# Performance work log

Hardware: AMD Instinct MI355X
Metric: run time of the kernel (lower is better)

The kernel has to match this reference:

```python
import jax, jax.numpy as jnp
import numpy as np

N_F, N_C = 100000, 25000          # fine / coarse node counts
C_IN, C_OUT = 128, 128
E_POOL, E = 200000, 400000        # pooling edges, coarse point-point edges


def setup_inputs() -> dict:
    key = jax.random.key(0)
    ks = jax.random.split(key, 12)
    x = jax.random.normal(ks[0], (N_F, C_IN), jnp.float32)
    # pooling edges: src in fine graph, dst in coarse graph
    pool_src = jax.random.randint(ks[1], (E_POOL,), 0, N_F, dtype=jnp.int64)
    pool_dst = jax.random.randint(ks[2], (E_POOL,), 0, N_C, dtype=jnp.int64)
    pool_edge_index = jnp.stack([pool_src, pool_dst])
    pool_edge_attr = jax.random.uniform(ks[3], (E_POOL,), jnp.float32)
    # coarse point-point edges
    src = jax.random.randint(ks[4], (E,), 0, N_C, dtype=jnp.int64)
    dst = jax.random.randint(ks[5], (E,), 0, N_C, dtype=jnp.int64)
    edge_index = jnp.stack([src, dst])
    edge_attr = jax.random.uniform(ks[6], (E,), jnp.float32)
    s_in = 1.0 / np.sqrt(C_IN).astype(np.float32)
    s_out = 1.0 / np.sqrt(C_OUT).astype(np.float32)
    W1_root = jax.random.normal(ks[7], (C_IN, C_OUT), jnp.float32) * s_in
    W1_nb = jax.random.normal(ks[8], (C_IN, C_OUT), jnp.float32) * s_in
    b1 = jnp.zeros((C_OUT,), jnp.float32)
    W2_root = jax.random.normal(ks[9], (C_OUT, C_OUT), jnp.float32) * s_out
    W2_nb = jax.random.normal(ks[10], (C_OUT, C_OUT), jnp.float32) * s_out
    b2 = jnp.zeros((C_OUT,), jnp.float32)
    return {
        "x": x,
        "pool_edge_index": pool_edge_index,
        "pool_edge_attr": pool_edge_attr,
        "edge_index": edge_index,
        "edge_attr": edge_attr,
        "W1_root": W1_root, "W1_nb": W1_nb, "b1": b1,
        "W2_root": W2_root, "W2_nb": W2_nb, "b2": b2,
        "n_coarse": N_C,
    }


def _graph_conv(h, edge_index, edge_attr, W_root, W_nb, b, n_nodes):
    # GraphConv with edge weights: out = h @ W_root + scatter_add(w_e * (h[src] @ W_nb), dst) + b
    msg = edge_attr[:, None] * (h[edge_index[0]] @ W_nb)          # [E, C_out]
    agg = jax.ops.segment_sum(msg, edge_index[1], num_segments=n_nodes)
    return h @ W_root + agg + b


def reference(x, pool_edge_index, pool_edge_attr, edge_index, edge_attr,
              W1_root, W1_nb, b1, W2_root, W2_nb, b2, n_coarse):
    # CustomPoolingAdd: weighted scatter-add fine -> coarse
    pooled = jax.ops.segment_sum(pool_edge_attr[:, None] * x[pool_edge_index[0]],
                                 pool_edge_index[1], num_segments=n_coarse)  # [N_c, C_in]
    h = _graph_conv(pooled, edge_index, edge_attr, W1_root, W1_nb, b1, n_coarse)
    h = _graph_conv(h, edge_index, edge_attr, W2_root, W2_nb, b2, n_coarse)
    return h
```

## Files before the change

### kernel.cpp

```cpp
#include <hip/hip_runtime.h>

typedef __attribute__((ext_vector_type(8))) short   short8;
typedef __attribute__((ext_vector_type(8))) __bf16  bf16x8;
typedef __attribute__((ext_vector_type(4))) float   f32x4;

__device__ __forceinline__ float bf2f(unsigned short u) {
    union { unsigned int i; float f; } v; v.i = ((unsigned int)u) << 16; return v.f;
}
__device__ __forceinline__ unsigned short f2bf(float f) {
    union { float f; unsigned int i; } v; v.f = f;
    unsigned int r = v.i + 0x7fffu + ((v.i >> 16) & 1u);
    return (unsigned short)(r >> 16);
}

__device__ __forceinline__ int load_idx(const void* p, int is64, long long i) {
    return is64 ? (int)((const long long*)p)[i] : ((const int*)p)[i];
}
__device__ __forceinline__ float load_f(const void* p, int isbf, long long i) {
    return isbf ? bf2f(((const unsigned short*)p)[i]) : ((const float*)p)[i];
}

__device__ __forceinline__ int self_is64(const int* p) {
    int lane = threadIdx.x & 63;
    unsigned long long b = __ballot(p[2 * lane + 1] != 0);
    return b == 0ull;
}
__device__ __forceinline__ int self_isbf(const unsigned int* p) {
    int lane = threadIdx.x & 63;
    unsigned int lo = p[lane] & 0xFFFFu;
    int e = (int)((lo >> 7) & 0xFF);
    int ok = (lo == 0u) || (e >= 88 && e <= 141);
    return (__ballot(!ok) == 0ull) ? 1 : 0;
}

__global__ void detect_kernel(const int* __restrict__ pei, const int* __restrict__ ei,
                              const unsigned int* f0, const unsigned int* f1,
                              const unsigned int* f2, const unsigned int* f3,
                              const unsigned int* f4, const unsigned int* f5,
                              const unsigned int* f6, const unsigned int* f7,
                              const unsigned int* f8,
                              int* __restrict__ flags) {
    int lane = threadIdx.x & 63;
    unsigned long long ba = __ballot(pei[2 * lane + 1] != 0);
    unsigned long long bb = __ballot(ei[2 * lane + 1] != 0);
    const unsigned int* fa[9] = {f0, f1, f2, f3, f4, f5, f6, f7, f8};
    int bf[9];
    #pragma unroll
    for (int t = 0; t < 9; t++) {
        unsigned int lo = fa[t][lane] & 0xFFFFu;
        int e = (int)((lo >> 7) & 0xFF);
        int ok = (lo == 0u) || (e >= 88 && e <= 141);
        bf[t] = (__ballot(!ok) == 0ull) ? 1 : 0;
    }
    if (lane == 0) {
        flags[0] = (ba == 0ull);
        flags[1] = (bb == 0ull);
        #pragma unroll
        for (int t = 0; t < 9; t++) flags[2 + t] = bf[t];
    }
}

#define PBKT_CAP 32
#define CBKT_CAP 64
#define OVF_CAP 4096

__global__ void fillpack_kernel(const void* __restrict__ pei, const void* __restrict__ pattr,
                                const void* __restrict__ ei, const void* __restrict__ eattr,
                                int* __restrict__ pcnt, int2* __restrict__ pbkt,
                                int* __restrict__ povfc, int4* __restrict__ povf,
                                int* __restrict__ ccnt, int2* __restrict__ cbkt,
                                int* __restrict__ covfc, int4* __restrict__ covf,
                                int Ep, int Ec, int gE,
                                const void* __restrict__ w1r, const void* __restrict__ w1n,
                                const void* __restrict__ w2r, const void* __restrict__ w2n,
                                unsigned short* __restrict__ wpack,
                                const void* __restrict__ x, unsigned short* __restrict__ xb,
                                long long elemsX) {
    int bid = (int)blockIdx.x;
    if (bid >= gE + 256) {
        int xisbf = self_isbf((const unsigned int*)x);
        if (xisbf) return;
        long long gid = (long long)(bid - gE - 256) * 256 + threadIdx.x;
        long long row = gid >> 3;
        int part = (int)(gid & 7);
        long long NF = elemsX >> 7;
        if (row >= NF) return;
        const float4* src = (const float4*)((const float*)x + row * 128 + part * 16);
        float4 a = src[0], b = src[1], c = src[2], d = src[3];
        uint4 o0, o1;
        o0.x = (unsigned int)f2bf(a.x) | ((unsigned int)f2bf(a.y) << 16);
        o0.y = (unsigned int)f2bf(a.z) | ((unsigned int)f2bf(a.w) << 16);
        o0.z = (unsigned int)f2bf(b.x) | ((unsigned int)f2bf(b.y) << 16);
        o0.w = (unsigned int)f2bf(b.z) | ((unsigned int)f2bf(b.w) << 16);
        o1.x = (unsigned int)f2bf(c.x) | ((unsigned int)f2bf(c.y) << 16);
        o1.y = (unsigned int)f2bf(c.z) | ((unsigned int)f2bf(c.w) << 16);
        o1.z = (unsigned int)f2bf(d.x) | ((unsigned int)f2bf(d.y) << 16);
        o1.w = (unsigned int)f2bf(d.z) | ((unsigned int)f2bf(d.w) << 16);
        uint4* dst = (uint4*)(xb + row * 128 + part * 16);
        dst[0] = o0; dst[1] = o1;
        return;
    }
    if (bid >= gE) {
        int gid = (bid - gE) * 256 + threadIdx.x;
        int layer = gid >> 15;
        int r = gid & 32767;
        int j = r & 7, lane = (r >> 3) & 63, ch = (r >> 9) & 7, ct = (r >> 12) & 7;
        int n = ct * 16 + (lane & 15);
        int k = ch * 32 + (lane >> 4) * 8 + j;
        const void* w;
        if (layer == 0) w = (k < 128) ? w1r : w1n;
        else            w = (k < 128) ? w2r : w2n;
        int fs = self_isbf((const unsigned int*)w);
        float v = load_f(w, fs, (long long)(k & 127) * 128 + n);
        wpack[gid] = f2bf(v);
        return;
    }
    long long g = (long long)bid * 256 + threadIdx.x;
    if (g < Ep) {
        int is64 = self_is64((const int*)pei);
        int abf = self_isbf((const unsigned int*)pattr);
        int s = load_idx(pei, is64, g);
        int d = load_idx(pei, is64, (long long)Ep + g);
        float w = load_f(pattr, abf, g);
        int pos = atomicAdd(&pcnt[d], 1);
        if (pos < PBKT_CAP) {
            pbkt[(long long)d * PBKT_CAP + pos] = make_int2(s, __float_as_int(w));
        } else {
            int oi = atomicAdd(povfc, 1);
            if (oi < OVF_CAP) povf[oi] = make_int4(s, __float_as_int(w), d, 0);
        }
    } else if (g - Ep < Ec) {
        long long e = g - Ep;
        int is64 = self_is64((const int*)ei);
        int abf = self_isbf((const unsigned int*)eattr);
        int s = load_idx(ei, is64, e);
        int d = load_idx(ei, is64, (long long)Ec + e);
        float w = load_f(eattr, abf, e);
        int pos = atomicAdd(&ccnt[d], 1);
        if (pos < CBKT_CAP) {
            cbkt[(long long)d * CBKT_CAP + pos] = make_int2(s, __float_as_int(w));
        } else {
            int oi = atomicAdd(covfc, 1);
            if (oi < OVF_CAP) covf[oi] = make_int4(s, __float_as_int(w), d, 0);
        }
    }
}

__global__ void gatherx_kernel(const void* __restrict__ x,
                               const unsigned short* __restrict__ xb, int haveXb,
                               const int* __restrict__ cnt,
                               const int2* __restrict__ bkt,
                               const int* __restrict__ ovfc,
                               const int4* __restrict__ ovf,
                               unsigned short* __restrict__ out, int NC) {
    int d = blockIdx.x * 4 + (threadIdx.x >> 6);
    if (d >= NC) return;
    int lane = threadIdx.x & 63;
    int j1 = cnt[d]; if (j1 > PBKT_CAP) j1 = PBKT_CAP;
    const int2* row = bkt + (long long)d * PBKT_CAP;
    float ax = 0.f, ay = 0.f;
    int xisbf = self_isbf((const unsigned int*)x);
    if (xisbf || haveXb) {
        const unsigned int* uin = xisbf ? (const unsigned int*)x : (const unsigned int*)xb;
        int j = 0;
        for (; j + 4 <= j1; j += 4) {
            int2 e0 = row[j], e1 = row[j + 1], e2 = row[j + 2], e3 = row[j + 3];
            unsigned int v0 = uin[(long long)e0.x * 64 + lane];
            unsigned int v1 = uin[(long long)e1.x * 64 + lane];
            unsigned int v2 = uin[(long long)e2.x * 64 + lane];
            unsigned int v3 = uin[(long long)e3.x * 64 + lane];
            ax += __int_as_float(e0.y) * bf2f((unsigned short)v0)
                + __int_as_float(e1.y) * bf2f((unsigned short)v1)
                + __int_as_float(e2.y) * bf2f((unsigned short)v2)
                + __int_as_float(e3.y) * bf2f((unsigned short)v3);
            ay += __int_as_float(e0.y) * bf2f((unsigned short)(v0 >> 16))
                + __int_as_float(e1.y) * bf2f((unsigned short)(v1 >> 16))
                + __int_as_float(e2.y) * bf2f((unsigned short)(v2 >> 16))
                + __int_as_float(e3.y) * bf2f((unsigned short)(v3 >> 16));
        }
        for (; j < j1; j++) {
            int2 e = row[j];
            float w = __int_as_float(e.y);
            unsigned int v = uin[(long long)e.x * 64 + lane];
            ax += w * bf2f((unsigned short)v);
            ay += w * bf2f((unsigned short)(v >> 16));
        }
        int novf = *ovfc;
        if (novf > 0) {
            if (novf > OVF_CAP) novf = OVF_CAP;
            for (int k = 0; k < novf; k++) {
                int4 e = ovf[k];
                if (e.z == d) {
                    float w = __int_as_float(e.y);
                    unsigned int v = uin[(long long)e.x * 64 + lane];
                    ax += w * bf2f((unsigned short)v);
                    ay += w * bf2f((unsigned short)(v >> 16));
                }
            }
        }
    } else {
        const float* fin = (const float*)x;
        int c0 = lane * 2;
        int j = 0;
        for (; j + 4 <= j1; j += 4) {
            int2 e0 = row[j], e1 = row[j + 1], e2 = row[j + 2], e3 = row[j + 3];
            float2 v0 = *(const float2*)(fin + (long long)e0.x * 128 + c0);
            float2 v1 = *(const float2*)(fin + (long long)e1.x * 128 + c0);
            float2 v2 = *(const float2*)(fin + (long long)e2.x * 128 + c0);
            float2 v3 = *(const float2*)(fin + (long long)e3.x * 128 + c0);
            ax += __int_as_float(e0.y) * v0.x + __int_as_float(e1.y) * v1.x
                + __int_as_float(e2.y) * v2.x + __int_as_float(e3.y) * v3.x;
            ay += __int_as_float(e0.y) * v0.y + __int_as_float(e1.y) * v1.y
                + __int_as_float(e2.y) * v2.y + __int_as_float(e3.y) * v3.y;
        }
        for (; j < j1; j++) {
            int2 e = row[j];
            float w = __int_as_float(e.y);
            float2 v = *(const float2*)(fin + (long long)e.x * 128 + c0);
            ax += w * v.x; ay += w * v.y;
        }
        int novf = *ovfc;
        if (novf > 0) {
            if (novf > OVF_CAP) novf = OVF_CAP;
            for (int k = 0; k < novf; k++) {
                int4 e = ovf[k];
                if (e.z == d) {
                    float w = __int_as_float(e.y);
                    float2 v = *(const float2*)(fin + (long long)e.x * 128 + c0);
                    ax += w * v.x; ay += w * v.y;
                }
            }
        }
    }
    unsigned int o = (unsigned int)f2bf(ax) | ((unsigned int)f2bf(ay) << 16);
    ((unsigned int*)out)[(long long)d * 64 + lane] = o;
}

__global__ void gatherb_kernel(const unsigned short* __restrict__ in,
                               const int* __restrict__ cnt,
                               const int2* __restrict__ bkt, int cap,
                               const int* __restrict__ ovfc,
                               const int4* __restrict__ ovf,
                               unsigned short* __restrict__ out, int NC) {
    int d = blockIdx.x * 4 + (threadIdx.x >> 6);
    if (d >= NC) return;
    int lane = threadIdx.x & 63;
    int j1 = cnt[d]; if (j1 > cap) j1 = cap;
    const int2* row = bkt + (long long)d * cap;
    float ax = 0.f, ay = 0.f;
    const unsigned int* uin = (const unsigned int*)in;
    int j = 0;
    for (; j + 8 <= j1; j += 8) {
        int2 e0 = row[j], e1 = row[j + 1], e2 = row[j + 2], e3 = row[j + 3];
        int2 e4 = row[j + 4], e5 = row[j + 5], e6 = row[j + 6], e7 = row[j + 7];
        unsigned int v0 = uin[(long long)e0.x * 64 + lane];
        unsigned int v1 = uin[(long long)e1.x * 64 + lane];
        unsigned int v2 = uin[(long long)e2.x * 64 + lane];
        unsigned int v3 = uin[(long long)e3.x * 64 + lane];
        unsigned int v4 = uin[(long long)e4.x * 64 + lane];
        unsigned int v5 = uin[(long long)e5.x * 64 + lane];
        unsigned int v6 = uin[(long long)e6.x * 64 + lane];
        unsigned int v7 = uin[(long long)e7.x * 64 + lane];
        ax += __int_as_float(e0.y) * bf2f((unsigned short)v0)
            + __int_as_float(e1.y) * bf2f((unsigned short)v1)
            + __int_as_float(e2.y) * bf2f((unsigned short)v2)
            + __int_as_float(e3.y) * bf2f((unsigned short)v3)
            + __int_as_float(e4.y) * bf2f((unsigned short)v4)
            + __int_as_float(e5.y) * bf2f((unsigned short)v5)
            + __int_as_float(e6.y) * bf2f((unsigned short)v6)
            + __int_as_float(e7.y) * bf2f((unsigned short)v7);
        ay += __int_as_float(e0.y) * bf2f((unsigned short)(v0 >> 16))
            + __int_as_float(e1.y) * bf2f((unsigned short)(v1 >> 16))
            + __int_as_float(e2.y) * bf2f((unsigned short)(v2 >> 16))
            + __int_as_float(e3.y) * bf2f((unsigned short)(v3 >> 16))
            + __int_as_float(e4.y) * bf2f((unsigned short)(v4 >> 16))
            + __int_as_float(e5.y) * bf2f((unsigned short)(v5 >> 16))
            + __int_as_float(e6.y) * bf2f((unsigned short)(v6 >> 16))
            + __int_as_float(e7.y) * bf2f((unsigned short)(v7 >> 16));
    }
    for (; j + 4 <= j1; j += 4) {
        int2 e0 = row[j], e1 = row[j + 1], e2 = row[j + 2], e3 = row[j + 3];
        unsigned int v0 = uin[(long long)e0.x * 64 + lane];
        unsigned int v1 = uin[(long long)e1.x * 64 + lane];
        unsigned int v2 = uin[(long long)e2.x * 64 + lane];
        unsigned int v3 = uin[(long long)e3.x * 64 + lane];
        ax += __int_as_float(e0.y) * bf2f((unsigned short)v0)
            + __int_as_float(e1.y) * bf2f((unsigned short)v1)
            + __int_as_float(e2.y) * bf2f((unsigned short)v2)
            + __int_as_float(e3.y) * bf2f((unsigned short)v3);
        ay += __int_as_float(e0.y) * bf2f((unsigned short)(v0 >> 16))
            + __int_as_float(e1.y) * bf2f((unsigned short)(v1 >> 16))
            + __int_as_float(e2.y) * bf2f((unsigned short)(v2 >> 16))
            + __int_as_float(e3.y) * bf2f((unsigned short)(v3 >> 16));
    }
    for (; j < j1; j++) {
        int2 e = row[j];
        float w = __int_as_float(e.y);
        unsigned int v = uin[(long long)e.x * 64 + lane];
        ax += w * bf2f((unsigned short)v);
        ay += w * bf2f((unsigned short)(v >> 16));
    }
    int novf = *ovfc;
    if (novf > 0) {
        if (novf > OVF_CAP) novf = OVF_CAP;
        for (int k = 0; k < novf; k++) {
            int4 e = ovf[k];
            if (e.z == d) {
                float w = __int_as_float(e.y);
                unsigned int v = uin[(long long)e.x * 64 + lane];
                ax += w * bf2f((unsigned short)v);
                ay += w * bf2f((unsigned short)(v >> 16));
            }
        }
    }
    unsigned int o = (unsigned int)f2bf(ax) | ((unsigned int)f2bf(ay) << 16);
    ((unsigned int*)out)[(long long)d * 64 + lane] = o;
}

__global__ __launch_bounds__(256, 4)
void gemm_mfma_kernel(const unsigned short* __restrict__ H,
                      const unsigned short* __restrict__ G,
                      const unsigned short* __restrict__ wpack,
                      const void* __restrict__ bias,
                      float* __restrict__ outF, unsigned short* __restrict__ outB,
                      int NC) {
    __shared__ unsigned short ldsA[64 * 264];
    int tid = threadIdx.x;
    long long r0 = (long long)blockIdx.x * 64;
    for (int i = tid; i < 4096; i += 256) {
        int mat = i >> 11;
        int flat = i & 2047;
        int row = flat >> 5;
        int c4 = flat & 31;
        long long r = r0 + row;
        const unsigned short* srcp = mat ? G : H;
        uint2 v = make_uint2(0u, 0u);
        if (r < NC) v = *(const uint2*)(srcp + r * 128 + c4 * 4);
        *(uint2*)&ldsA[row * 264 + mat * 128 + c4 * 4] = v;
    }
    __syncthreads();

    int wave = tid >> 6, lane = tid & 63;
    int m = lane & 15, quad = lane >> 4;
    int arow = wave * 16 + m;

    bf16x8 a[8];
    #pragma unroll
    for (int ch = 0; ch < 8; ch++) {
        short8 av = *(const short8*)&ldsA[arow * 264 + ch * 32 + quad * 8];
        a[ch] = __builtin_bit_cast(bf16x8, av);
    }

    f32x4 acc[8];
    #pragma unroll
    for (int ct = 0; ct < 8; ct++) acc[ct] = (f32x4){0.f, 0.f, 0.f, 0.f};

    #pragma unroll
    for (int ct = 0; ct < 8; ct++) {
        #pragma unroll
        for (int ch = 0; ch < 8; ch++) {
            short8 bv = *(const short8*)(wpack + ((ct * 8 + ch) * 64 + lane) * 8);
            acc[ct] = __builtin_amdgcn_mfma_f32_16x16x32_bf16(
                a[ch], __builtin_bit_cast(bf16x8, bv), acc[ct], 0, 0, 0);
        }
    }

    int bbf = self_isbf((const unsigned int*)bias);
    #pragma unroll
    for (int ct = 0; ct < 8; ct++) {
        int n = ct * 16 + m;
        float bv = load_f(bias, bbf, n);
        #pragma unroll
        for (int r = 0; r < 4; r++) {
            long long rr = r0 + wave * 16 + quad * 4 + r;
            if (rr < NC) {
                float val = acc[ct][r] + bv;
                if (outF) outF[rr * 128 + n] = val;
                else      outB[rr * 128 + n] = f2bf(val);
            }
        }
    }
}

__global__ void pool_scatter_kernel(const void* __restrict__ x, const void* __restrict__ pei,
                                    const void* __restrict__ pattr, const int* __restrict__ flags,
                                    float* __restrict__ pooled, int Ep, int CI) {
    int c = blockIdx.y * blockDim.x + threadIdx.x;
    if (c >= CI) return;
    int e = blockIdx.x;
    int is64 = flags[0], xbf = flags[2], abf = flags[3];
    int s = load_idx(pei, is64, e);
    int d = load_idx(pei, is64, (long long)Ep + e);
    float w = load_f(pattr, abf, e);
    float v = load_f(x, xbf, (long long)s * CI + c);
    atomicAdd(&pooled[(long long)d * CI + c], w * v);
}

__global__ void conv_scatter_kernel(const float* __restrict__ t, const void* __restrict__ ei,
                                    const void* __restrict__ attr, const int* __restrict__ flags,
                                    float* __restrict__ outacc, int Ec, int CO) {
    int c = blockIdx.y * blockDim.x + threadIdx.x;
    if (c >= CO) return;
    int e = blockIdx.x;
    int is64 = flags[1], abf = flags[4];
    int s = load_idx(ei, is64, e);
    int d = load_idx(ei, is64, (long long)Ec + e);
    float w = load_f(attr, abf, e);
    atomicAdd(&outacc[(long long)d * CO + c], w * t[(long long)s * CO + c]);
}

__global__ void gemm_kernel(const float* H, const void* __restrict__ Wr,
                            const void* __restrict__ Wn, const void* __restrict__ bias,
                            const int* __restrict__ flags, int fWr, int fWn, int fB,
                            float* out_root, float* out_t, int NC, int CI, int CO) {
    __shared__ float lds[4][1024];
    int wave = threadIdx.x >> 6;
    int lane = threadIdx.x & 63;
    int r = blockIdx.x * 4 + wave;
    if (r < NC) {
        const float* hrow = H + (long long)r * CI;
        for (int k = lane; k < CI; k += 64) lds[wave][k] = hrow[k];
    }
    __syncthreads();
    if (r >= NC) return;
    int wrbf = flags[fWr], wnbf = flags[fWn], bbf = flags[fB];
    for (int c0 = lane * 2; c0 < CO; c0 += 128) {
        int two = (c0 + 1 < CO);
        float ar0 = 0.f, ar1 = 0.f, an0 = 0.f, an1 = 0.f;
        for (int k = 0; k < CI; k++) {
            float h = lds[wave][k];
            ar0 += h * load_f(Wr, wrbf, (long long)k * CO + c0);
            an0 += h * load_f(Wn, wnbf, (long long)k * CO + c0);
            if (two) {
                ar1 += h * load_f(Wr, wrbf, (long long)k * CO + c0 + 1);
                an1 += h * load_f(Wn, wnbf, (long long)k * CO + c0 + 1);
            }
        }
        long long o = (long long)r * CO + c0;
        out_root[o] = ar0 + load_f(bias, bbf, c0);
        out_t[o] = an0;
        if (two) {
            out_root[o + 1] = ar1 + load_f(bias, bbf, c0 + 1);
            out_t[o + 1] = an1;
        }
    }
}

__global__ void to_out_kernel(const float* __restrict__ in, float* __restrict__ out, long long n) {
    long long stride = (long long)gridDim.x * blockDim.x;
    for (long long i = (long long)blockIdx.x * blockDim.x + threadIdx.x; i < n; i += stride)
        out[i] = in[i];
}

extern "C" void kernel_launch(void* const* d_in, const int* in_sizes, int n_in,
                              void* d_out, int out_size, void* d_ws, size_t ws_size,
                              hipStream_t stream) {
    const void* x = d_in[0]; const void* pei = d_in[1]; const void* pattr = d_in[2];
    const void* ei = d_in[3]; const void* eattr = d_in[4];
    const void* w1r = d_in[5]; const void* w1n = d_in[6]; const void* b1 = d_in[7];
    const void* w2r = d_in[8]; const void* w2n = d_in[9]; const void* b2 = d_in[10];

    long long CO = in_sizes[7];
    long long CI = CO > 0 ? in_sizes[5] / CO : 0;
    long long Ep = in_sizes[2];
    long long Ec = in_sizes[4];
    long long NC = CO > 0 ? (long long)out_size / CO : 0;
    int sane = (CO > 0 && CI > 0 && CI <= 1024 && CO <= 1024 &&
                CI * CO == in_sizes[5] && NC * CO == out_size &&
                Ep > 0 && Ec > 0 && in_sizes[0] % CI == 0);
    if (!sane) { CO = 128; CI = 128; Ep = 200000; Ec = 400000; NC = 25000; }

    char* ws = (char*)d_ws;

    if (CI == 128 && CO == 128) {
        long long elemsX = in_sizes[0];
        size_t off = 0;
        unsigned short* bufP = (unsigned short*)(ws + off); off += (size_t)NC * 128 * 2;
        unsigned short* bufH = (unsigned short*)(ws + off); off += (size_t)NC * 128 * 2;
        unsigned short* bufG = (unsigned short*)(ws + off); off += (size_t)NC * 128 * 2;
        unsigned short* wpack = (unsigned short*)(ws + off); off += 65536 * 2;
        int* pcnt  = (int*)(ws + off); off += NC * 4;
        int* ccnt  = (int*)(ws + off); off += NC * 4;
        int* povfc = (int*)(ws + off); off += 4;
        int* covfc = (int*)(ws + off); off += 4;
        off = (off + 15) & ~(size_t)15;
        int4* povf = (int4*)(ws + off); off += (size_t)OVF_CAP * 16;
        int4* covf = (int4*)(ws + off); off += (size_t)OVF_CAP * 16;
        int2* pbkt = (int2*)(ws + off); off += (size_t)NC * PBKT_CAP * 8;
        int2* cbkt = (int2*)(ws + off); off += (size_t)NC * CBKT_CAP * 8;
        off = (off + 15) & ~(size_t)15;
        unsigned short* xb = (unsigned short*)(ws + off);
        size_t xbBytes = (size_t)elemsX * 2;
        int haveXb = (off + xbBytes <= ws_size) ? 1 : 0;

        hipMemsetAsync(pcnt, 0, (2 * NC + 2) * 4, stream);

        int gE = (int)((Ep + Ec + 255) / 256);
        int gConv = haveXb ? (int)((elemsX / 16 + 255) / 256) : 0;
        fillpack_kernel<<<gE + 256 + gConv, 256, 0, stream>>>(
            pei, pattr, ei, eattr,
            pcnt, pbkt, povfc, povf,
            ccnt, cbkt, covfc, covf,
            (int)Ep, (int)Ec, gE,
            w1r, w1n, w2r, w2n, wpack,
            x, xb, elemsX);

        int gN4 = (int)((NC + 3) / 4);
        int gN64 = (int)((NC + 63) / 64);
        gatherx_kernel<<<gN4, 256, 0, stream>>>(x, xb, haveXb, pcnt, pbkt, povfc, povf,
                                                bufP, (int)NC);
        gatherb_kernel<<<gN4, 256, 0, stream>>>(bufP, ccnt, cbkt, CBKT_CAP, covfc, covf,
                                                bufG, (int)NC);
        gemm_mfma_kernel<<<gN64, 256, 0, stream>>>(bufP, bufG, wpack, b1,
                                                   nullptr, bufH, (int)NC);
        gatherb_kernel<<<gN4, 256, 0, stream>>>(bufH, ccnt, cbkt, CBKT_CAP, covfc, covf,
                                                bufG, (int)NC);
        gemm_mfma_kernel<<<gN64, 256, 0, stream>>>(bufH, bufG, wpack + 32768, b2,
                                                   (float*)d_out, nullptr, (int)NC);
        return;
    }

    size_t szP = (size_t)NC * CI * sizeof(float);
    size_t szO = (size_t)NC * CO * sizeof(float);
    float *bufP, *bufA, *bufB, *bufC; int* flags;
    if (CI == CO) {
        bufP = (float*)ws; bufA = (float*)(ws + szP);
        bufB = bufP; bufC = bufA;
        flags = (int*)(ws + szP + szO);
    } else {
        bufP = (float*)ws; bufA = (float*)(ws + szP);
        bufB = (float*)(ws + szP + szO); bufC = (float*)(ws + szP + 2 * szO);
        flags = (int*)(ws + szP + 3 * szO);
    }
    detect_kernel<<<1, 64, 0, stream>>>(
        (const int*)pei, (const int*)ei,
        (const unsigned int*)x, (const unsigned int*)pattr, (const unsigned int*)eattr,
        (const unsigned int*)w1r, (const unsigned int*)w1n, (const unsigned int*)b1,
        (const unsigned int*)w2r, (const unsigned int*)w2n, (const unsigned int*)b2,
        flags);
    hipMemsetAsync(bufP, 0, szP, stream);
    int blkP = (CI % 64 == 0 && CI <= 256) ? (int)CI : 256;
    int blkC = (CO % 64 == 0 && CO <= 256) ? (int)CO : 256;
    dim3 gP((unsigned)Ep, (unsigned)((CI + blkP - 1) / blkP));
    dim3 gC((unsigned)Ec, (unsigned)((CO + blkC - 1) / blkC));
    int gG = (int)((NC + 3) / 4);
    pool_scatter_kernel<<<gP, blkP, 0, stream>>>(x, pei, pattr, flags, bufP, (int)Ep, (int)CI);
    if (CI == CO) {
        gemm_kernel<<<gG, 256, 0, stream>>>(bufP, w1r, w1n, b1, flags, 5, 6, 7,
                                            bufA, bufP, (int)NC, (int)CI, (int)CO);
        conv_scatter_kernel<<<gC, blkC, 0, stream>>>(bufP, ei, eattr, flags, bufA, (int)Ec, (int)CO);
        gemm_kernel<<<gG, 256, 0, stream>>>(bufA, w2r, w2n, b2, flags, 8, 9, 10,
                                            bufP, bufA, (int)NC, (int)CO, (int)CO);
        conv_scatter_kernel<<<gC, blkC, 0, stream>>>(bufA, ei, eattr, flags, bufP, (int)Ec, (int)CO);
        to_out_kernel<<<4096, 256, 0, stream>>>(bufP, (float*)d_out, NC * CO);
    } else {
        gemm_kernel<<<gG, 256, 0, stream>>>(bufP, w1r, w1n, b1, flags, 5, 6, 7,
                                            bufA, bufB, (int)NC, (int)CI, (int)CO);
        conv_scatter_kernel<<<gC, blkC, 0, stream>>>(bufB, ei, eattr, flags, bufA, (int)Ec, (int)CO);
        gemm_kernel<<<gG, 256, 0, stream>>>(bufA, w2r, w2n, b2, flags, 8, 9, 10,
                                            bufB, bufC, (int)NC, (int)CO, (int)CO);
        conv_scatter_kernel<<<gC, blkC, 0, stream>>>(bufC, ei, eattr, flags, bufB, (int)Ec, (int)CO);
        to_out_kernel<<<4096, 256, 0, stream>>>(bufB, (float*)d_out, NC * CO);
    }
}
```

Baseline: 231.8 us.

## Fuse neighbor gather into MFMA GEMM and drop x bf16 pre-conversion

Merges the per-layer neighbor aggregation kernel into the GEMM kernel, so each block gathers its 64 rows' neighbor sums straight into LDS next to the root features and no longer writes and rereads an intermediate G buffer. It also removes the pass that converted x to bf16 inside the fill kernel, so gatherx now reads fp32 x directly when x is not already bf16. The trade-off is less parallelism in the fused gather (64 rows per block, 16 per wave, run serially), and gatherx moves twice the bytes on the fp32 path.

```diff
diff --git a/kernel.cpp b/kernel.cpp
--- a/kernel.cpp
+++ b/kernel.cpp
@@ -73,33 +73,8 @@
                                 int Ep, int Ec, int gE,
                                 const void* __restrict__ w1r, const void* __restrict__ w1n,
                                 const void* __restrict__ w2r, const void* __restrict__ w2n,
-                                unsigned short* __restrict__ wpack,
-                                const void* __restrict__ x, unsigned short* __restrict__ xb,
-                                long long elemsX) {
+                                unsigned short* __restrict__ wpack) {
     int bid = (int)blockIdx.x;
-    if (bid >= gE + 256) {
-        int xisbf = self_isbf((const unsigned int*)x);
-        if (xisbf) return;
-        long long gid = (long long)(bid - gE - 256) * 256 + threadIdx.x;
-        long long row = gid >> 3;
-        int part = (int)(gid & 7);
-        long long NF = elemsX >> 7;
-        if (row >= NF) return;
-        const float4* src = (const float4*)((const float*)x + row * 128 + part * 16);
-        float4 a = src[0], b = src[1], c = src[2], d = src[3];
-        uint4 o0, o1;
-        o0.x = (unsigned int)f2bf(a.x) | ((unsigned int)f2bf(a.y) << 16);
-        o0.y = (unsigned int)f2bf(a.z) | ((unsigned int)f2bf(a.w) << 16);
-        o0.z = (unsigned int)f2bf(b.x) | ((unsigned int)f2bf(b.y) << 16);
-        o0.w = (unsigned int)f2bf(b.z) | ((unsigned int)f2bf(b.w) << 16);
-        o1.x = (unsigned int)f2bf(c.x) | ((unsigned int)f2bf(c.y) << 16);
-        o1.y = (unsigned int)f2bf(c.z) | ((unsigned int)f2bf(c.w) << 16);
-        o1.z = (unsigned int)f2bf(d.x) | ((unsigned int)f2bf(d.y) << 16);
-        o1.w = (unsigned int)f2bf(d.z) | ((unsigned int)f2bf(d.w) << 16);
-        uint4* dst = (uint4*)(xb + row * 128 + part * 16);
-        dst[0] = o0; dst[1] = o1;
-        return;
-    }
     if (bid >= gE) {
         int gid = (bid - gE) * 256 + threadIdx.x;
         int layer = gid >> 15;
@@ -147,7 +122,6 @@
 }
 
 __global__ void gatherx_kernel(const void* __restrict__ x,
-                               const unsigned short* __restrict__ xb, int haveXb,
                                const int* __restrict__ cnt,
                                const int2* __restrict__ bkt,
                                const int* __restrict__ ovfc,
@@ -160,8 +134,8 @@
     const int2* row = bkt + (long long)d * PBKT_CAP;
     float ax = 0.f, ay = 0.f;
     int xisbf = self_isbf((const unsigned int*)x);
-    if (xisbf || haveXb) {
-        const unsigned int* uin = xisbf ? (const unsigned int*)x : (const unsigned int*)xb;
+    if (xisbf) {
+        const unsigned int* uin = (const unsigned int*)x;
         int j = 0;
         for (; j + 4 <= j1; j += 4) {
             int2 e0 = row[j], e1 = row[j + 1], e2 = row[j + 2], e3 = row[j + 3];
@@ -236,111 +210,108 @@
     ((unsigned int*)out)[(long long)d * 64 + lane] = o;
 }
 
-__global__ void gatherb_kernel(const unsigned short* __restrict__ in,
-                               const int* __restrict__ cnt,
-                               const int2* __restrict__ bkt, int cap,
-                               const int* __restrict__ ovfc,
-                               const int4* __restrict__ ovf,
-                               unsigned short* __restrict__ out, int NC) {
-    int d = blockIdx.x * 4 + (threadIdx.x >> 6);
-    if (d >= NC) return;
-    int lane = threadIdx.x & 63;
-    int j1 = cnt[d]; if (j1 > cap) j1 = cap;
-    const int2* row = bkt + (long long)d * cap;
-    float ax = 0.f, ay = 0.f;
-    const unsigned int* uin = (const unsigned int*)in;
-    int j = 0;
-    for (; j + 8 <= j1; j += 8) {
-        int2 e0 = row[j], e1 = row[j + 1], e2 = row[j + 2], e3 = row[j + 3];
-        int2 e4 = row[j + 4], e5 = row[j + 5], e6 = row[j + 6], e7 = row[j + 7];
-        unsigned int v0 = uin[(long long)e0.x * 64 + lane];
-        unsigned int v1 = uin[(long long)e1.x * 64 + lane];
-        unsigned int v2 = uin[(long long)e2.x * 64 + lane];
-        unsigned int v3 = uin[(long long)e3.x * 64 + lane];
-        unsigned int v4 = uin[(long long)e4.x * 64 + lane];
-        unsigned int v5 = uin[(long long)e5.x * 64 + lane];
-        unsigned int v6 = uin[(long long)e6.x * 64 + lane];
-        unsigned int v7 = uin[(long long)e7.x * 64 + lane];
-        ax += __int_as_float(e0.y) * bf2f((unsigned short)v0)
-            + __int_as_float(e1.y) * bf2f((unsigned short)v1)
-            + __int_as_float(e2.y) * bf2f((unsigned short)v2)
-            + __int_as_float(e3.y) * bf2f((unsigned short)v3)
-            + __int_as_float(e4.y) * bf2f((unsigned short)v4)
-            + __int_as_float(e5.y) * bf2f((unsigned short)v5)
-            + __int_as_float(e6.y) * bf2f((unsigned short)v6)
-            + __int_as_float(e7.y) * bf2f((unsigned short)v7);
-        ay += __int_as_float(e0.y) * bf2f((unsigned short)(v0 >> 16))
-            + __int_as_float(e1.y) * bf2f((unsigned short)(v1 >> 16))
-            + __int_as_float(e2.y) * bf2f((unsigned short)(v2 >> 16))
-            + __int_as_float(e3.y) * bf2f((unsigned short)(v3 >> 16))
-            + __int_as_float(e4.y) * bf2f((unsigned short)(v4 >> 16))
-            + __int_as_float(e5.y) * bf2f((unsigned short)(v5 >> 16))
-            + __int_as_float(e6.y) * bf2f((unsigned short)(v6 >> 16))
-            + __int_as_float(e7.y) * bf2f((unsigned short)(v7 >> 16));
-    }
-    for (; j + 4 <= j1; j += 4) {
-        int2 e0 = row[j], e1 = row[j + 1], e2 = row[j + 2], e3 = row[j + 3];
-        unsigned int v0 = uin[(long long)e0.x * 64 + lane];
-        unsigned int v1 = uin[(long long)e1.x * 64 + lane];
-        unsigned int v2 = uin[(long long)e2.x * 64 + lane];
-        unsigned int v3 = uin[(long long)e3.x * 64 + lane];
-        ax += __int_as_float(e0.y) * bf2f((unsigned short)v0)
-            + __int_as_float(e1.y) * bf2f((unsigned short)v1)
-            + __int_as_float(e2.y) * bf2f((unsigned short)v2)
-            + __int_as_float(e3.y) * bf2f((unsigned short)v3);
-        ay += __int_as_float(e0.y) * bf2f((unsigned short)(v0 >> 16))
-            + __int_as_float(e1.y) * bf2f((unsigned short)(v1 >> 16))
-            + __int_as_float(e2.y) * bf2f((unsigned short)(v2 >> 16))
-            + __int_as_float(e3.y) * bf2f((unsigned short)(v3 >> 16));
-    }
-    for (; j < j1; j++) {
-        int2 e = row[j];
-        float w = __int_as_float(e.y);
-        unsigned int v = uin[(long long)e.x * 64 + lane];
-        ax += w * bf2f((unsigned short)v);
-        ay += w * bf2f((unsigned short)(v >> 16));
-    }
-    int novf = *ovfc;
-    if (novf > 0) {
-        if (novf > OVF_CAP) novf = OVF_CAP;
-        for (int k = 0; k < novf; k++) {
-            int4 e = ovf[k];
-            if (e.z == d) {
+__global__ __launch_bounds__(256, 4)
+void gathergemm_kernel(const unsigned short* __restrict__ H,
+                       const int* __restrict__ cnt,
+                       const int2* __restrict__ bkt, int cap,
+                       const int* __restrict__ ovfc,
+                       const int4* __restrict__ ovf,
+                       const unsigned short* __restrict__ wpack,
+                       const void* __restrict__ bias,
+                       float* __restrict__ outF, unsigned short* __restrict__ outB,
+                       int NC) {
+    __shared__ unsigned short ldsA[64 * 264];
+    int tid = threadIdx.x;
+    long long r0 = (long long)blockIdx.x * 64;
+
+    for (int i = tid; i < 2048; i += 256) {
+        int row = i >> 5;
+        int c4 = i & 31;
+        long long r = r0 + row;
+        uint2 v = make_uint2(0u, 0u);
+        if (r < NC) v = *(const uint2*)(H + r * 128 + c4 * 4);
+        *(uint2*)&ldsA[row * 264 + c4 * 4] = v;
+    }
+
+    int wave = tid >> 6, lane = tid & 63;
+    const unsigned int* uin = (const unsigned int*)H;
+    for (int t = 0; t < 16; t++) {
+        int row = wave * 16 + t;
+        long long d = r0 + row;
+        float ax = 0.f, ay = 0.f;
+        if (d < NC) {
+            int j1 = cnt[d]; if (j1 > cap) j1 = cap;
+            const int2* brow = bkt + d * cap;
+            int j = 0;
+            for (; j + 8 <= j1; j += 8) {
+                int2 e0 = brow[j],     e1 = brow[j + 1], e2 = brow[j + 2], e3 = brow[j + 3];
+                int2 e4 = brow[j + 4], e5 = brow[j + 5], e6 = brow[j + 6], e7 = brow[j + 7];
+                unsigned int v0 = uin[(long long)e0.x * 64 + lane];
+                unsigned int v1 = uin[(long long)e1.x * 64 + lane];
+                unsigned int v2 = uin[(long long)e2.x * 64 + lane];
+                unsigned int v3 = uin[(long long)e3.x * 64 + lane];
+                unsigned int v4 = uin[(long long)e4.x * 64 + lane];
+                unsigned int v5 = uin[(long long)e5.x * 64 + lane];
+                unsigned int v6 = uin[(long long)e6.x * 64 + lane];
+                unsigned int v7 = uin[(long long)e7.x * 64 + lane];
+                ax += __int_as_float(e0.y) * bf2f((unsigned short)v0)
+                    + __int_as_float(e1.y) * bf2f((unsigned short)v1)
+                    + __int_as_float(e2.y) * bf2f((unsigned short)v2)
+                    + __int_as_float(e3.y) * bf2f((unsigned short)v3)
+                    + __int_as_float(e4.y) * bf2f((unsigned short)v4)
+                    + __int_as_float(e5.y) * bf2f((unsigned short)v5)
+                    + __int_as_float(e6.y) * bf2f((unsigned short)v6)
+                    + __int_as_float(e7.y) * bf2f((unsigned short)v7);
+                ay += __int_as_float(e0.y) * bf2f((unsigned short)(v0 >> 16))
+                    + __int_as_float(e1.y) * bf2f((unsigned short)(v1 >> 16))
+                    + __int_as_float(e2.y) * bf2f((unsigned short)(v2 >> 16))
+                    + __int_as_float(e3.y) * bf2f((unsigned short)(v3 >> 16))
+                    + __int_as_float(e4.y) * bf2f((unsigned short)(v4 >> 16))
+                    + __int_as_float(e5.y) * bf2f((unsigned short)(v5 >> 16))
+                    + __int_as_float(e6.y) * bf2f((unsigned short)(v6 >> 16))
+                    + __int_as_float(e7.y) * bf2f((unsigned short)(v7 >> 16));
+            }
+            for (; j + 4 <= j1; j += 4) {
+                int2 e0 = brow[j], e1 = brow[j + 1], e2 = brow[j + 2], e3 = brow[j + 3];
+                unsigned int v0 = uin[(long long)e0.x * 64 + lane];
+                unsigned int v1 = uin[(long long)e1.x * 64 + lane];
+                unsigned int v2 = uin[(long long)e2.x * 64 + lane];
+                unsigned int v3 = uin[(long long)e3.x * 64 + lane];
+                ax += __int_as_float(e0.y) * bf2f((unsigned short)v0)
+                    + __int_as_float(e1.y) * bf2f((unsigned short)v1)
+                    + __int_as_float(e2.y) * bf2f((unsigned short)v2)
+                    + __int_as_float(e3.y) * bf2f((unsigned short)v3);
+                ay += __int_as_float(e0.y) * bf2f((unsigned short)(v0 >> 16))
+                    + __int_as_float(e1.y) * bf2f((unsigned short)(v1 >> 16))
+                    + __int_as_float(e2.y) * bf2f((unsigned short)(v2 >> 16))
+                    + __int_as_float(e3.y) * bf2f((unsigned short)(v3 >> 16));
+            }
+            for (; j < j1; j++) {
+                int2 e = brow[j];
                 float w = __int_as_float(e.y);
                 unsigned int v = uin[(long long)e.x * 64 + lane];
                 ax += w * bf2f((unsigned short)v);
                 ay += w * bf2f((unsigned short)(v >> 16));
             }
-        }
-    }
-    unsigned int o = (unsigned int)f2bf(ax) | ((unsigned int)f2bf(ay) << 16);
-    ((unsigned int*)out)[(long long)d * 64 + lane] = o;
-}
-
-__global__ __launch_bounds__(256, 4)
-void gemm_mfma_kernel(const unsigned short* __restrict__ H,
-                      const unsigned short* __restrict__ G,
-                      const unsigned short* __restrict__ wpack,
-                      const void* __restrict__ bias,
-                      float* __restrict__ outF, unsigned short* __restrict__ outB,
-                      int NC) {
-    __shared__ unsigned short ldsA[64 * 264];
-    int tid = threadIdx.x;
-    long long r0 = (long long)blockIdx.x * 64;
-    for (int i = tid; i < 4096; i += 256) {
-        int mat = i >> 11;
-        int flat = i & 2047;
-        int row = flat >> 5;
-        int c4 = flat & 31;
-        long long r = r0 + row;
-        const unsigned short* srcp = mat ? G : H;
-        uint2 v = make_uint2(0u, 0u);
-        if (r < NC) v = *(const uint2*)(srcp + r * 128 + c4 * 4);
-        *(uint2*)&ldsA[row * 264 + mat * 128 + c4 * 4] = v;
+            int novf = *ovfc;
+            if (novf > 0) {
+                if (novf > OVF_CAP) novf = OVF_CAP;
+                for (int k = 0; k < novf; k++) {
+                    int4 e = ovf[k];
+                    if (e.z == d) {
+                        float w = __int_as_float(e.y);
+                        unsigned int v = uin[(long long)e.x * 64 + lane];
+                        ax += w * bf2f((unsigned short)v);
+                        ay += w * bf2f((unsigned short)(v >> 16));
+                    }
+                }
+            }
+        }
+        *(unsigned int*)&ldsA[row * 264 + 128 + lane * 2] =
+            (unsigned int)f2bf(ax) | ((unsigned int)f2bf(ay) << 16);
     }
     __syncthreads();
 
-    int wave = tid >> 6, lane = tid & 63;
     int m = lane & 15, quad = lane >> 4;
     int arow = wave * 16 + m;
 
@@ -473,11 +444,9 @@
     char* ws = (char*)d_ws;
 
     if (CI == 128 && CO == 128) {
-        long long elemsX = in_sizes[0];
         size_t off = 0;
         unsigned short* bufP = (unsigned short*)(ws + off); off += (size_t)NC * 128 * 2;
         unsigned short* bufH = (unsigned short*)(ws + off); off += (size_t)NC * 128 * 2;
-        unsigned short* bufG = (unsigned short*)(ws + off); off += (size_t)NC * 128 * 2;
         unsigned short* wpack = (unsigned short*)(ws + off); off += 65536 * 2;
         int* pcnt  = (int*)(ws + off); off += NC * 4;
         int* ccnt  = (int*)(ws + off); off += NC * 4;
@@ -488,35 +457,25 @@
         int4* covf = (int4*)(ws + off); off += (size_t)OVF_CAP * 16;
         int2* pbkt = (int2*)(ws + off); off += (size_t)NC * PBKT_CAP * 8;
         int2* cbkt = (int2*)(ws + off); off += (size_t)NC * CBKT_CAP * 8;
-        off = (off + 15) & ~(size_t)15;
-        unsigned short* xb = (unsigned short*)(ws + off);
-        size_t xbBytes = (size_t)elemsX * 2;
-        int haveXb = (off + xbBytes <= ws_size) ? 1 : 0;
 
         hipMemsetAsync(pcnt, 0, (2 * NC + 2) * 4, stream);
 
         int gE = (int)((Ep + Ec + 255) / 256);
-        int gConv = haveXb ? (int)((elemsX / 16 + 255) / 256) : 0;
-        fillpack_kernel<<<gE + 256 + gConv, 256, 0, stream>>>(
+        fillpack_kernel<<<gE + 256, 256, 0, stream>>>(
             pei, pattr, ei, eattr,
             pcnt, pbkt, povfc, povf,
             ccnt, cbkt, covfc, covf,
             (int)Ep, (int)Ec, gE,
-            w1r, w1n, w2r, w2n, wpack,
-            x, xb, elemsX);
+            w1r, w1n, w2r, w2n, wpack);
 
         int gN4 = (int)((NC + 3) / 4);
         int gN64 = (int)((NC + 63) / 64);
-        gatherx_kernel<<<gN4, 256, 0, stream>>>(x, xb, haveXb, pcnt, pbkt, povfc, povf,
-                                                bufP, (int)NC);
-        gatherb_kernel<<<gN4, 256, 0, stream>>>(bufP, ccnt, cbkt, CBKT_CAP, covfc, covf,
-                                                bufG, (int)NC);
-        gemm_mfma_kernel<<<gN64, 256, 0, stream>>>(bufP, bufG, wpack, b1,
-                                                   nullptr, bufH, (int)NC);
-        gatherb_kernel<<<gN4, 256, 0, stream>>>(bufH, ccnt, cbkt, CBKT_CAP, covfc, covf,
-                                                bufG, (int)NC);
-        gemm_mfma_kernel<<<gN64, 256, 0, stream>>>(bufH, bufG, wpack + 32768, b2,
-                                                   (float*)d_out, nullptr, (int)NC);
+        gatherx_kernel<<<gN4, 256, 0, stream>>>(x, pcnt, pbkt, povfc, povf, bufP, (int)NC);
+        gathergemm_kernel<<<gN64, 256, 0, stream>>>(bufP, ccnt, cbkt, CBKT_CAP, covfc, covf,
+                                                    wpack, b1, nullptr, bufH, (int)NC);
+        gathergemm_kernel<<<gN64, 256, 0, stream>>>(bufH, ccnt, cbkt, CBKT_CAP, covfc, covf,
+                                                    wpack + 32768, b2,
+                                                    (float*)d_out, nullptr, (int)NC);
         return;
     }
 
```

Result: slower. 281.7 us (+21.6%).
